# Kernel tuning notes

Measured on AMD Instinct MI355X. Metric: run time of the kernel, lower is better.

The kernel has to match this reference:

```python
import jax, jax.numpy as jnp
import numpy as np

B, S, NH, D_IN = 64, 512, 4, 256   # batch, seq_len, rnn n_head, input_dim
H = 256                            # hidden_dim == attention activation_dim
AH = 256                           # attention_hidden_dim (attn out_dim)
OUT = 3                            # output_dim (sentiment classes)


def setup_inputs() -> dict:
    key = jax.random.key(0)
    ks = jax.random.split(key, 9)
    def p(k, shape, scale=0.05):
        return jax.random.normal(k, shape, dtype=jnp.float32) * scale
    return dict(
        x=jax.random.normal(ks[0], (B, S, NH, D_IN), dtype=jnp.float32),
        Wk=p(ks[1], (D_IN, H)), bk=jnp.zeros((H,), jnp.float32),
        Wq=p(ks[2], (H, H)),    bq=jnp.zeros((H,), jnp.float32),
        w_mlp=p(ks[3], (2 * H,)),
        Wproj=p(ks[4], (H, AH)), bproj=jnp.zeros((AH,), jnp.float32),
        W1=p(ks[5], (D_IN + AH, H)), b1=jnp.zeros((H,), jnp.float32),
        W2=p(ks[6], (H, H)),    b2=jnp.zeros((H,), jnp.float32),
        Wo=p(ks[7], (NH * H, OUT)), bo=jnp.zeros((OUT,), jnp.float32),
    )


def _cell(x_t, hidden, params):
    Wk, bk, Wq, bq, w_mlp, Wproj, bproj, W1, b1, W2, b2, Wo, bo = params
    kx = x_t @ Wk + bk           # [B, NH, H]  keys from step input
    qx = hidden @ Wq + bq        # [B, NH, H]  queries from hidden state
    w1, w2 = w_mlp[:H], w_mlp[H:]
    # MLP score: s[b,i,j] = tanh(cat(kx[b,j], qx[b,i]) . w) = tanh(kx[b,j].w1 + qx[b,i].w2)
    score = jnp.tanh((qx @ w2)[:, :, None] + (kx @ w1)[:, None, :])  # [B, NH, NH]
    score = jax.nn.softmax(score, axis=-1)
    attn = jnp.einsum('bij,bjh->bih', score, kx) @ Wproj + bproj     # [B, NH, AH]
    concat = jnp.concatenate([x_t, attn], axis=-1)                   # [B, NH, D_IN+AH]
    hidden_new = jax.nn.relu(concat @ W1 + b1) @ W2 + b2             # [B, NH, H]
    logits = hidden_new.reshape(B, NH * H) @ Wo + bo                 # [B, OUT]
    out = jax.nn.log_softmax(logits, axis=-1)
    return out, hidden_new


def reference(x, Wk, bk, Wq, bq, w_mlp, Wproj, bproj, W1, b1, W2, b2, Wo, bo):
    params = (Wk, bk, Wq, bq, w_mlp, Wproj, bproj, W1, b1, W2, b2, Wo, bo)
    h0 = jnp.zeros((B, NH, H), x.dtype)
    xs = jnp.swapaxes(x, 0, 1)  # [S, B, NH, D_IN] for scan over time
    def step(h, x_t):
        out, h_new = _cell(x_t, h, params)
        return h_new, out
    h_final, outs = jax.lax.scan(step, h0, xs)
    # return_sequence=False: last-step log-softmax output and final hidden
    return outs[-1], h_final
```

## Files before the change

kernel.cpp:

```cpp
#include <hip/hip_runtime.h>
#include <hip/hip_bf16.h>
#include <math.h>

#define BB   64
#define SS   512
#define NHH  4
#define DD   256
#define HH   256
#define LDH  264

typedef __attribute__((ext_vector_type(8))) short  short8;
typedef __attribute__((ext_vector_type(4))) float  floatx4;


__device__ __forceinline__ unsigned short f2b(float f) {
  __hip_bfloat16 h = __float2bfloat16(f);
  return __builtin_bit_cast(unsigned short, h);
}
__device__ __forceinline__ float b2f(unsigned short u) {
  unsigned v = (unsigned)u << 16;
  return __builtin_bit_cast(float, v);
}

__global__ __launch_bounds__(256) void init_kernel(
    const float* __restrict__ Wk, const float* __restrict__ Wproj,
    const float* __restrict__ W1, const float* __restrict__ Wq,
    const float* __restrict__ bq, const float* __restrict__ w_mlp,
    const float* __restrict__ bproj, const float* __restrict__ W2,
    const float* __restrict__ b2, float* __restrict__ ws,
    unsigned short* __restrict__ wpack)
{
  __shared__ float vsh[256];
  __shared__ float red[256];
  int tid = threadIdx.x;

  if (blockIdx.x > 0) {
    int idx = (blockIdx.x - 1) * 256 + tid;
    int mat = idx >> 16;
    int rem = idx & 65535;
    int j    = rem & 7;
    int lane = (rem >> 3) & 63;
    int ks   = (rem >> 9) & 7;
    int pan  = rem >> 12;
    int k = ks * 32 + ((lane >> 4) << 3) + j;
    int n = pan * 16 + (lane & 15);
    float v;
    if      (mat == 0) v = Wk[k * 256 + n];
    else if (mat == 1) v = W1[k * 256 + n];
    else if (mat == 2) v = Wproj[k * 256 + n];
    else               v = W1[(256 + k) * 256 + n];
    wpack[idx] = f2b(v);
    return;
  }

  const float* w2 = w_mlp + HH;
  {
    float a = 0.f;
    const float4* Wq4 = (const float4*)(Wq + tid * 256);
    const float4* w24 = (const float4*)w2;
    for (int k = 0; k < 64; ++k) {
      float4 wv = Wq4[k], xv = w24[k];
      a = fmaf(wv.x, xv.x, fmaf(wv.y, xv.y, fmaf(wv.z, xv.z, fmaf(wv.w, xv.w, a))));
    }
    vsh[tid] = a;
  }
  __syncthreads();
  {
    float a2 = 0.f;
    const float4* W24 = (const float4*)(W2 + tid * 256);
    const float4* v4  = (const float4*)vsh;
    for (int k = 0; k < 64; ++k) {
      float4 wv = W24[k], xv = v4[k];
      a2 = fmaf(wv.x, xv.x, fmaf(wv.y, xv.y, fmaf(wv.z, xv.z, fmaf(wv.w, xv.w, a2))));
    }
    ws[tid] = a2;
  }
  {
    float a3 = 0.f;
    for (int k = 0; k < 256; ++k) a3 = fmaf(bproj[k], W1[(256 + k) * 256 + tid], a3);
    ws[256 + tid] = a3;
  }
  red[tid] = bq[tid] * w2[tid];
  __syncthreads();
  for (int s = 128; s; s >>= 1) { if (tid < s) red[tid] += red[tid + s]; __syncthreads(); }
  float c = red[0];
  __syncthreads();
  ws[768 + tid] = c;
  red[tid] = b2[tid] * vsh[tid];
  __syncthreads();
  for (int s = 128; s; s >>= 1) { if (tid < s) red[tid] += red[tid + s]; __syncthreads(); }
  if (tid == 0) ws[512] = red[0] + c;
}

__device__ __forceinline__ void mfma_gemm4(
    const unsigned short* A_lds, const short8* __restrict__ Bp,
    const float* __restrict__ bias, floatx4 acc[4][4], int l, int w)
{
  int col = l & 15, quad = l >> 4;
#pragma unroll
  for (int pp = 0; pp < 4; ++pp) {
    float bv = bias ? bias[(w * 4 + pp) * 16 + col] : 0.f;
#pragma unroll
    for (int mf = 0; mf < 4; ++mf)
      acc[mf][pp] = (floatx4){bv, bv, bv, bv};
  }
  const short8* Bb = Bp + (size_t)(w * 4) * 512 + l;
  short8 bb[3][4];
  short8 aa[2][4];
#pragma unroll
  for (int pp = 0; pp < 4; ++pp) bb[0][pp] = Bb[pp * 512];
#pragma unroll
  for (int pp = 0; pp < 4; ++pp) bb[1][pp] = Bb[pp * 512 + 64];
#pragma unroll
  for (int mf = 0; mf < 4; ++mf)
    aa[0][mf] = *(const short8*)(A_lds + (mf * 16 + col) * LDH + quad * 8);
#pragma unroll
  for (int kb = 0; kb < 8; ++kb) {
    if (kb + 2 < 8) {
#pragma unroll
      for (int pp = 0; pp < 4; ++pp)
        bb[(kb + 2) % 3][pp] = Bb[pp * 512 + (kb + 2) * 64];
    }
    if (kb + 1 < 8) {
#pragma unroll
      for (int mf = 0; mf < 4; ++mf)
        aa[(kb + 1) & 1][mf] =
            *(const short8*)(A_lds + (mf * 16 + col) * LDH + (kb + 1) * 32 + quad * 8);
    }
#pragma unroll
    for (int mf = 0; mf < 4; ++mf)
#pragma unroll
      for (int pp = 0; pp < 4; ++pp)
        acc[mf][pp] = __builtin_amdgcn_mfma_f32_16x16x32_bf16(
            aa[kb & 1][mf], bb[kb % 3][pp], acc[mf][pp], 0, 0, 0);
  }
}

__device__ __forceinline__ void acc_to_lds(
    unsigned short* D, const floatx4 acc[4][4], int l, int w)
{
  int col = l & 15, quad = l >> 4;
#pragma unroll
  for (int mf = 0; mf < 4; ++mf)
#pragma unroll
    for (int pp = 0; pp < 4; ++pp)
#pragma unroll
      for (int r = 0; r < 4; ++r)
        D[(mf * 16 + quad * 4 + r) * LDH + (w * 4 + pp) * 16 + col] = f2b(acc[mf][pp][r]);
}

__device__ __forceinline__ void acc_to_global(
    unsigned short* __restrict__ dst, const floatx4 acc[4][4],
    int l, int w, int b, int tt)
{
  int col = l & 15, quad = l >> 4;
#pragma unroll
  for (int mf = 0; mf < 4; ++mf)
#pragma unroll
    for (int r = 0; r < 4; ++r) {
      int m2 = mf * 16 + quad * 4 + r;
      size_t base = (((size_t)(tt * 16 + (m2 >> 2)) * 64 + b) * 4 + (m2 & 3)) * 256;
#pragma unroll
      for (int pp = 0; pp < 4; ++pp)
        dst[base + (w * 4 + pp) * 16 + col] = f2b(acc[mf][pp][r]);
    }
}

__device__ void precompute_block(
    int px, const float* __restrict__ x, const unsigned short* __restrict__ wpack,
    const float* __restrict__ bk, const float* __restrict__ b1,
    const float* __restrict__ w_mlp,
    float* __restrict__ kw_c, unsigned short* __restrict__ xw1_c,
    unsigned short* __restrict__ kpw_c, int t0, char* smem)
{
  float* kwbuf = (float*)smem;
  unsigned short* XS = (unsigned short*)(smem + 2048);
  unsigned short* TS = XS + 64 * LDH;

  int b  = px & 63;
  int tt = px >> 6;
  int tid = threadIdx.x;
  int l = tid & 63, w = tid >> 6;
  int col = l & 15, quad = l >> 4;

  const float4* xsrc = (const float4*)(x + (size_t)(b * SS + t0 + tt * 16) * NHH * DD);
#pragma unroll
  for (int i = 0; i < 16; ++i) {
    int f4 = i * 256 + tid;
    int r = f4 >> 6, c4 = f4 & 63;
    float4 v = xsrc[f4];
    ushort4 h;
    h.x = f2b(v.x); h.y = f2b(v.y); h.z = f2b(v.z); h.w = f2b(v.w);
    *(ushort4*)&XS[r * LDH + c4 * 4] = h;
  }
  __syncthreads();

  const short8* wp0 = (const short8*)(wpack);
  const short8* wp1 = (const short8*)(wpack + 65536);
  const short8* wp2 = (const short8*)(wpack + 2 * 65536);
  const short8* wp3 = (const short8*)(wpack + 3 * 65536);

  floatx4 acc[4][4];

  mfma_gemm4(XS, wp0, bk, acc, l, w);
  acc_to_lds(TS, acc, l, w);
  __syncthreads();

  {
    float part = 0.f;
    const unsigned short* trow = TS + l * LDH + w * 64;
#pragma unroll
    for (int j8 = 0; j8 < 8; ++j8) {
      short8 tv = *(const short8*)(trow + j8 * 8);
#pragma unroll
      for (int j = 0; j < 8; ++j)
        part = fmaf(b2f((unsigned short)tv[j]), w_mlp[w * 64 + j8 * 8 + j], part);
    }
    kwbuf[l * 4 + w] = part;
  }

  mfma_gemm4(XS, wp1, b1, acc, l, w);
  __syncthreads();
  if (tid < 64) {
    float s = kwbuf[tid * 4] + kwbuf[tid * 4 + 1] + kwbuf[tid * 4 + 2] + kwbuf[tid * 4 + 3];
    kw_c[((size_t)(tt * 16 + (tid >> 2)) * 64 + b) * 4 + (tid & 3)] = s;
  }
  acc_to_global(xw1_c, acc, l, w, b, tt);

  mfma_gemm4(TS, wp2, nullptr, acc, l, w);
  acc_to_lds(XS, acc, l, w);
  __syncthreads();

  mfma_gemm4(XS, wp3, nullptr, acc, l, w);
  acc_to_global(kpw_c, acc, l, w, b, tt);
}

__device__ __forceinline__ float wave_reduce_sum(float x) {
#define DPPSTEP(ctrl, rmask)                                                   \
  {                                                                            \
    int _s = __builtin_amdgcn_update_dpp(0, __builtin_bit_cast(int, x),        \
                                         (ctrl), (rmask), 0xf, true);          \
    x += __builtin_bit_cast(float, _s);                                        \
  }
  DPPSTEP(0x111, 0xf)
  DPPSTEP(0x112, 0xf)
  DPPSTEP(0x114, 0xf)
  DPPSTEP(0x118, 0xf)
  DPPSTEP(0x142, 0xa)
  DPPSTEP(0x143, 0xc)
#undef DPPSTEP
  return __builtin_bit_cast(float, __builtin_amdgcn_readlane(__builtin_bit_cast(int, x), 63));
}

__device__ __forceinline__ float tanh_fast(float y) {
  float ex = __expf(2.f * y);
  return 1.f - 2.f * __builtin_amdgcn_rcpf(ex + 1.f);
}

__device__ void seq_block(
    const unsigned short* __restrict__ xw1_c, const unsigned short* __restrict__ kpw_c,
    const float* __restrict__ kw_c, float* __restrict__ ws,
    float* __restrict__ relu_u, int t0, int n)
{
  int b = blockIdx.x;
  int tid = threadIdx.x;
  int i = tid >> 6, l = tid & 63;

  float4 v2v = ((const float4*)ws)[l];
  float4 cbv = ((const float4*)(ws + 256))[l];
  float c2 = ws[512];
  float qw = ws[768 + b * 4 + i];

  const ushort4* xw = (const ushort4*)xw1_c;
  const ushort4* kp = (const ushort4*)kpw_c;

  struct Slot { ushort4 x, k0, k1, k2, k3; float4 kw; };

  auto load = [&](Slot& s, int tc) {
    size_t rb_ = (size_t)(tc * 64 + b) * 4;
    s.x  = xw[(rb_ + i) * 64 + l];
    s.k0 = kp[(rb_ + 0) * 64 + l];
    s.k1 = kp[(rb_ + 1) * 64 + l];
    s.k2 = kp[(rb_ + 2) * 64 + l];
    s.k3 = kp[(rb_ + 3) * 64 + l];
    s.kw = *(const float4*)&kw_c[rb_];
  };

  auto step = [&](Slot& s, int t) {
    float e0 = tanh_fast(qw + s.kw.x);
    float e1 = tanh_fast(qw + s.kw.y);
    float e2 = tanh_fast(qw + s.kw.z);
    float e3 = tanh_fast(qw + s.kw.w);
    float q0 = __expf(e0), q1 = __expf(e1), q2 = __expf(e2), q3 = __expf(e3);
    float inv = __builtin_amdgcn_rcpf(q0 + q1 + q2 + q3);
    float4 K0 = {b2f(s.k0.x), b2f(s.k0.y), b2f(s.k0.z), b2f(s.k0.w)};
    float4 K1 = {b2f(s.k1.x), b2f(s.k1.y), b2f(s.k1.z), b2f(s.k1.w)};
    float4 K2 = {b2f(s.k2.x), b2f(s.k2.y), b2f(s.k2.z), b2f(s.k2.w)};
    float4 K3 = {b2f(s.k3.x), b2f(s.k3.y), b2f(s.k3.z), b2f(s.k3.w)};
    float4 X  = {b2f(s.x.x) + cbv.x, b2f(s.x.y) + cbv.y,
                 b2f(s.x.z) + cbv.z, b2f(s.x.w) + cbv.w};
    float4 a;
    a.x = fmaf(q0, K0.x, fmaf(q1, K1.x, fmaf(q2, K2.x, q3 * K3.x)));
    a.y = fmaf(q0, K0.y, fmaf(q1, K1.y, fmaf(q2, K2.y, q3 * K3.y)));
    a.z = fmaf(q0, K0.z, fmaf(q1, K1.z, fmaf(q2, K2.z, q3 * K3.z)));
    a.w = fmaf(q0, K0.w, fmaf(q1, K1.w, fmaf(q2, K2.w, q3 * K3.w)));
    float4 u;
    u.x = fmaf(a.x, inv, X.x); u.y = fmaf(a.y, inv, X.y);
    u.z = fmaf(a.z, inv, X.z); u.w = fmaf(a.w, inv, X.w);
    float4 r;
    r.x = fmaxf(u.x, 0.f); r.y = fmaxf(u.y, 0.f);
    r.z = fmaxf(u.z, 0.f); r.w = fmaxf(u.w, 0.f);
    float d = fmaf(r.x, v2v.x, fmaf(r.y, v2v.y, fmaf(r.z, v2v.z, r.w * v2v.w)));
    qw = wave_reduce_sum(d) + c2;
    if (t0 + t == SS - 1)
      *(float4*)&relu_u[(size_t)(b * 4 + i) * 256 + l * 4] = r;
  };

  Slot s0, s1, s2, s3;
  load(s0, 0); load(s1, 1); load(s2, 2); load(s3, 3);
  for (int t = 0; t < n; t += 4) {
    int nt;
    step(s0, t);     nt = t + 4; load(s0, nt < n ? nt : n - 1);
    step(s1, t + 1); nt = t + 5; load(s1, nt < n ? nt : n - 1);
    step(s2, t + 2); nt = t + 6; load(s2, nt < n ? nt : n - 1);
    step(s3, t + 3); nt = t + 7; load(s3, nt < n ? nt : n - 1);
  }
  if (l == 0) ws[768 + b * 4 + i] = qw;
}

__global__ __launch_bounds__(256, 2) void fused_kernel(
    const float* __restrict__ x, const unsigned short* __restrict__ wpack,
    const float* __restrict__ bk, const float* __restrict__ b1,
    const float* __restrict__ w_mlp,
    float* kwB, unsigned short* xw1B, unsigned short* kpwB, int t0_pre,
    const float* kwA, const unsigned short* xw1A, const unsigned short* kpwA,
    int t0_seq, int n_seq,
    float* __restrict__ ws, float* __restrict__ relu_u)
{
  __shared__ __align__(16) char smem[2048 + 2 * 64 * LDH * 2];
  if (blockIdx.x < 64) {
    if (n_seq > 0) seq_block(xw1A, kpwA, kwA, ws, relu_u, t0_seq, n_seq);
    return;
  }
  precompute_block(blockIdx.x - 64, x, wpack, bk, b1, w_mlp,
                   kwB, xw1B, kpwB, t0_pre, smem);
}

__global__ __launch_bounds__(256) void final_hidden_kernel(
    const float* __restrict__ relu_u, const float* __restrict__ W2,
    const float* __restrict__ b2, float* __restrict__ out)
{
  __shared__ float rs[256];
  int row = blockIdx.x;
  int tid = threadIdx.x;
  rs[tid] = relu_u[(size_t)row * 256 + tid];
  __syncthreads();
  float acc = b2[tid];
  for (int k = 0; k < 256; ++k) acc = fmaf(rs[k], W2[k * 256 + tid], acc);
  out[192 + (size_t)row * 256 + tid] = acc;
}

__global__ __launch_bounds__(256) void final_logits_kernel(
    const float* __restrict__ hf, const float* __restrict__ Wo,
    const float* __restrict__ bo, float* __restrict__ outp)
{
  __shared__ float r0[256], r1[256], r2[256];
  int b = blockIdx.x;
  int tid = threadIdx.x;
  float a0 = 0.f, a1 = 0.f, a2 = 0.f;
  for (int k = tid; k < 1024; k += 256) {
    float h = hf[(size_t)b * 1024 + k];
    a0 = fmaf(h, Wo[k * 3 + 0], a0);
    a1 = fmaf(h, Wo[k * 3 + 1], a1);
    a2 = fmaf(h, Wo[k * 3 + 2], a2);
  }
  r0[tid] = a0; r1[tid] = a1; r2[tid] = a2;
  __syncthreads();
  for (int s = 128; s; s >>= 1) {
    if (tid < s) { r0[tid] += r0[tid + s]; r1[tid] += r1[tid + s]; r2[tid] += r2[tid + s]; }
    __syncthreads();
  }
  if (tid == 0) {
    float l0 = r0[0] + bo[0], l1 = r1[0] + bo[1], l2 = r2[0] + bo[2];
    float m = fmaxf(l0, fmaxf(l1, l2));
    float lse = m + logf(expf(l0 - m) + expf(l1 - m) + expf(l2 - m));
    outp[b * 3 + 0] = l0 - lse;
    outp[b * 3 + 1] = l1 - lse;
    outp[b * 3 + 2] = l2 - lse;
  }
}

extern "C" void kernel_launch(void* const* d_in, const int* in_sizes, int n_in,
                              void* d_out, int out_size, void* d_ws, size_t ws_size,
                              hipStream_t stream)
{
  const float* x     = (const float*)d_in[0];
  const float* Wk    = (const float*)d_in[1];
  const float* bk    = (const float*)d_in[2];
  const float* Wq    = (const float*)d_in[3];
  const float* bq    = (const float*)d_in[4];
  const float* w_mlp = (const float*)d_in[5];
  const float* Wproj = (const float*)d_in[6];
  const float* bproj = (const float*)d_in[7];
  const float* W1    = (const float*)d_in[8];
  const float* b1    = (const float*)d_in[9];
  const float* W2    = (const float*)d_in[10];
  const float* b2    = (const float*)d_in[11];
  const float* Wo    = (const float*)d_in[12];
  const float* bo    = (const float*)d_in[13];
  float* out = (float*)d_out;
  float* ws  = (float*)d_ws;

  float* ru = ws + 1024;
  unsigned short* wpack = (unsigned short*)(ws + 66560);
  const size_t OFF_CH = 66560 + 131072;
  const long per_t = 256 + 65536;

  long ws_floats = (long)(ws_size / 4);
  long avail = ws_floats - (long)OFF_CH;

  int Tc = 128;
  while (Tc > 0 && 2L * Tc * per_t > avail) Tc -= 16;
  bool pipelined = (Tc >= 16);
  if (!pipelined) {
    Tc = 128;
    while (Tc > 16 && (long)Tc * per_t > avail) Tc -= 16;
  }

  float* bufA = ws + OFF_CH;
  float* bufB = pipelined ? bufA + (size_t)Tc * per_t : bufA;

  auto kw_of  = [&](float* base) { return base; };
  auto xw_of  = [&](float* base) { return (unsigned short*)(base + (size_t)Tc * 256); };
  auto kpw_of = [&](float* base) { return (unsigned short*)(base + (size_t)Tc * 256) + (size_t)Tc * 65536; };

  init_kernel<<<1025, 256, 0, stream>>>(Wk, Wproj, W1, Wq, bq, w_mlp, bproj, W2, b2,
                                        ws, wpack);

  int C = (SS + Tc - 1) / Tc;

  if (pipelined) {
    for (int r = 0; r <= C; ++r) {
      bool hasPre = (r < C);
      bool hasSeq = (r >= 1);
      int t0p = r * Tc;
      int np  = hasPre ? ((SS - t0p) < Tc ? (SS - t0p) : Tc) : 0;
      int t0s = (r - 1) * Tc;
      int ns  = hasSeq ? ((SS - t0s) < Tc ? (SS - t0s) : Tc) : 0;
      float* pB = ((r & 1) ? bufB : bufA);
      float* pA = (((r - 1) & 1) ? bufB : bufA);
      int grid = 64 + (hasPre ? 64 * (np / 16) : 0);
      fused_kernel<<<grid, 256, 0, stream>>>(
          x, wpack, bk, b1, w_mlp,
          kw_of(pB), xw_of(pB), kpw_of(pB), t0p,
          kw_of(pA), xw_of(pA), kpw_of(pA), t0s, ns,
          ws, ru);
    }
  } else {
    for (int c = 0; c < C; ++c) {
      int t0 = c * Tc;
      int n = (SS - t0) < Tc ? (SS - t0) : Tc;
      fused_kernel<<<64 + 64 * (n / 16), 256, 0, stream>>>(
          x, wpack, bk, b1, w_mlp,
          kw_of(bufA), xw_of(bufA), kpw_of(bufA), t0,
          kw_of(bufA), xw_of(bufA), kpw_of(bufA), 0, 0,
          ws, ru);
      fused_kernel<<<64, 256, 0, stream>>>(
          x, wpack, bk, b1, w_mlp,
          kw_of(bufA), xw_of(bufA), kpw_of(bufA), t0,
          kw_of(bufA), xw_of(bufA), kpw_of(bufA), t0, n,
          ws, ru);
    }
  }

  final_hidden_kernel<<<BB * NHH, 256, 0, stream>>>(ru, W2, b2, out);
  final_logits_kernel<<<BB, 256, 0, stream>>>(out + 192, Wo, bo, out);
}
```

Measured before the change: 427.8 us.

## Fold Wk·Wproj·W1b into one fused weight to cut precompute GEMMs

Precomputes the product Wk·Wproj·W1[256:] (and the folded biases and Wk·w1) in new init kernels, so each precompute block runs two MFMA GEMMs on x instead of four chained ones. This also removes the intermediate LDS tile and its syncs, shrinking shared memory enough to raise the occupancy hint to 3 blocks. The A-fragment double buffering in the GEMM loop is dropped in favour of per-iteration loads. Folding three matrices in fp32, then rounding the product to bf16, changes rounding behaviour slightly, and init now costs three launches.

```diff
diff --git a/kernel.cpp b/kernel.cpp
--- a/kernel.cpp
+++ b/kernel.cpp
@@ -12,6 +12,19 @@
 typedef __attribute__((ext_vector_type(8))) short  short8;
 typedef __attribute__((ext_vector_type(4))) float  floatx4;
 
+#define OFF_V2     0
+#define OFF_CB1    256
+#define OFF_C2     512
+#define OFF_CKW    513
+#define OFF_QW     768
+#define OFF_WK1    1024
+#define OFF_BKP    1280
+#define OFF_VT     1536
+#define OFF_RU     1792
+#define OFF_WFUSE  67328
+#define OFF_WKF    132864
+#define OFF_PACK   198400
+#define OFF_CH     263936
 
 __device__ __forceinline__ unsigned short f2b(float f) {
   __hip_bfloat16 h = __float2bfloat16(f);
@@ -22,74 +35,121 @@
   return __builtin_bit_cast(float, v);
 }
 
-__global__ __launch_bounds__(256) void init_kernel(
-    const float* __restrict__ Wk, const float* __restrict__ Wproj,
-    const float* __restrict__ W1, const float* __restrict__ Wq,
-    const float* __restrict__ bq, const float* __restrict__ w_mlp,
-    const float* __restrict__ bproj, const float* __restrict__ W2,
-    const float* __restrict__ b2, float* __restrict__ ws,
-    unsigned short* __restrict__ wpack)
-{
-  __shared__ float vsh[256];
-  __shared__ float red[256];
+__global__ __launch_bounds__(256) void initA_kernel(
+    const float* __restrict__ Wproj, const float* __restrict__ W1,
+    const float* __restrict__ bk, const float* __restrict__ bproj,
+    const float* __restrict__ Wq, const float* __restrict__ w_mlp,
+    float* __restrict__ ws)
+{
   int tid = threadIdx.x;
-
-  if (blockIdx.x > 0) {
-    int idx = (blockIdx.x - 1) * 256 + tid;
-    int mat = idx >> 16;
-    int rem = idx & 65535;
-    int j    = rem & 7;
-    int lane = (rem >> 3) & 63;
-    int ks   = (rem >> 9) & 7;
-    int pan  = rem >> 12;
-    int k = ks * 32 + ((lane >> 4) << 3) + j;
-    int n = pan * 16 + (lane & 15);
-    float v;
-    if      (mat == 0) v = Wk[k * 256 + n];
-    else if (mat == 1) v = W1[k * 256 + n];
-    else if (mat == 2) v = Wproj[k * 256 + n];
-    else               v = W1[(256 + k) * 256 + n];
-    wpack[idx] = f2b(v);
-    return;
-  }
-
-  const float* w2 = w_mlp + HH;
-  {
+  int bx = blockIdx.x;
+  const float* W1b = W1 + 256 * 256;
+  if (bx < 256) {
+    __shared__ float row[256];
+    row[tid] = Wproj[bx * 256 + tid];
+    __syncthreads();
+    float acc = 0.f;
+#pragma unroll 8
+    for (int k = 0; k < 256; ++k)
+      acc = fmaf(row[k], W1b[k * 256 + tid], acc);
+    ws[OFF_WFUSE + bx * 256 + tid] = acc;
+  } else if (bx == 256) {
+    float acc = bproj[tid];
+#pragma unroll 8
+    for (int k = 0; k < 256; ++k)
+      acc = fmaf(bk[k], Wproj[k * 256 + tid], acc);
+    ws[OFF_BKP + tid] = acc;
+  } else {
+    const float4* Wq4 = (const float4*)(Wq + tid * 256);
+    const float4* w24 = (const float4*)(w_mlp + 256);
     float a = 0.f;
-    const float4* Wq4 = (const float4*)(Wq + tid * 256);
-    const float4* w24 = (const float4*)w2;
     for (int k = 0; k < 64; ++k) {
       float4 wv = Wq4[k], xv = w24[k];
       a = fmaf(wv.x, xv.x, fmaf(wv.y, xv.y, fmaf(wv.z, xv.z, fmaf(wv.w, xv.w, a))));
     }
-    vsh[tid] = a;
-  }
-  __syncthreads();
-  {
-    float a2 = 0.f;
-    const float4* W24 = (const float4*)(W2 + tid * 256);
-    const float4* v4  = (const float4*)vsh;
+    ws[OFF_VT + tid] = a;
+  }
+}
+
+__global__ __launch_bounds__(256) void initB_kernel(
+    const float* __restrict__ Wk, const float* __restrict__ W1,
+    const float* __restrict__ b1, const float* __restrict__ W2,
+    const float* __restrict__ b2, const float* __restrict__ bq,
+    const float* __restrict__ bk, const float* __restrict__ w_mlp,
+    float* __restrict__ ws)
+{
+  int tid = threadIdx.x;
+  int bx = blockIdx.x;
+  if (bx < 256) {
+    __shared__ float row[256];
+    row[tid] = Wk[bx * 256 + tid];
+    __syncthreads();
+    float acc = 0.f;
+    const float* Wf = ws + OFF_WFUSE;
+#pragma unroll 8
+    for (int k = 0; k < 256; ++k)
+      acc = fmaf(row[k], Wf[k * 256 + tid], acc);
+    ws[OFF_WKF + bx * 256 + tid] = acc;
+  } else if (bx == 256) {
+    const float* W1b = W1 + 256 * 256;
+    float acc = b1[tid];
+#pragma unroll 8
+    for (int k = 0; k < 256; ++k)
+      acc = fmaf(ws[OFF_BKP + k], W1b[k * 256 + tid], acc);
+    ws[OFF_CB1 + tid] = acc;
+  } else if (bx == 257) {
+    __shared__ float red[256];
+    {
+      const float4* W24 = (const float4*)(W2 + tid * 256);
+      const float4* v4  = (const float4*)(ws + OFF_VT);
+      float a = 0.f;
+      for (int k = 0; k < 64; ++k) {
+        float4 wv = W24[k], xv = v4[k];
+        a = fmaf(wv.x, xv.x, fmaf(wv.y, xv.y, fmaf(wv.z, xv.z, fmaf(wv.w, xv.w, a))));
+      }
+      ws[OFF_V2 + tid] = a;
+    }
+    red[tid] = bq[tid] * w_mlp[256 + tid];
+    __syncthreads();
+    for (int s = 128; s; s >>= 1) { if (tid < s) red[tid] += red[tid + s]; __syncthreads(); }
+    float s2 = red[0];
+    __syncthreads();
+    ws[OFF_QW + tid] = s2;
+    red[tid] = b2[tid] * ws[OFF_VT + tid];
+    __syncthreads();
+    for (int s = 128; s; s >>= 1) { if (tid < s) red[tid] += red[tid + s]; __syncthreads(); }
+    if (tid == 0) ws[OFF_C2] = red[0] + s2;
+    __syncthreads();
+    red[tid] = bk[tid] * w_mlp[tid];
+    __syncthreads();
+    for (int s = 128; s; s >>= 1) { if (tid < s) red[tid] += red[tid + s]; __syncthreads(); }
+    if (tid == 0) ws[OFF_CKW] = red[0];
+  } else {
+    const float4* Wk4 = (const float4*)(Wk + tid * 256);
+    const float4* w14 = (const float4*)(w_mlp);
+    float a = 0.f;
     for (int k = 0; k < 64; ++k) {
-      float4 wv = W24[k], xv = v4[k];
-      a2 = fmaf(wv.x, xv.x, fmaf(wv.y, xv.y, fmaf(wv.z, xv.z, fmaf(wv.w, xv.w, a2))));
-    }
-    ws[tid] = a2;
-  }
-  {
-    float a3 = 0.f;
-    for (int k = 0; k < 256; ++k) a3 = fmaf(bproj[k], W1[(256 + k) * 256 + tid], a3);
-    ws[256 + tid] = a3;
-  }
-  red[tid] = bq[tid] * w2[tid];
-  __syncthreads();
-  for (int s = 128; s; s >>= 1) { if (tid < s) red[tid] += red[tid + s]; __syncthreads(); }
-  float c = red[0];
-  __syncthreads();
-  ws[768 + tid] = c;
-  red[tid] = b2[tid] * vsh[tid];
-  __syncthreads();
-  for (int s = 128; s; s >>= 1) { if (tid < s) red[tid] += red[tid + s]; __syncthreads(); }
-  if (tid == 0) ws[512] = red[0] + c;
+      float4 wv = Wk4[k], xv = w14[k];
+      a = fmaf(wv.x, xv.x, fmaf(wv.y, xv.y, fmaf(wv.z, xv.z, fmaf(wv.w, xv.w, a))));
+    }
+    ws[OFF_WK1 + tid] = a;
+  }
+}
+
+__global__ __launch_bounds__(256) void initC_kernel(
+    const float* __restrict__ W1, float* __restrict__ ws)
+{
+  int idx = blockIdx.x * 256 + threadIdx.x;
+  int mat = idx >> 16;
+  int rem = idx & 65535;
+  int j    = rem & 7;
+  int lane = (rem >> 3) & 63;
+  int ks   = (rem >> 9) & 7;
+  int pan  = rem >> 12;
+  int k = ks * 32 + ((lane >> 4) << 3) + j;
+  int n = pan * 16 + (lane & 15);
+  float v = (mat == 0) ? ws[OFF_WKF + k * 256 + n] : W1[k * 256 + n];
+  ((unsigned short*)(ws + OFF_PACK))[idx] = f2b(v);
 }
 
 __device__ __forceinline__ void mfma_gemm4(
@@ -106,14 +166,10 @@
   }
   const short8* Bb = Bp + (size_t)(w * 4) * 512 + l;
   short8 bb[3][4];
-  short8 aa[2][4];
 #pragma unroll
   for (int pp = 0; pp < 4; ++pp) bb[0][pp] = Bb[pp * 512];
 #pragma unroll
   for (int pp = 0; pp < 4; ++pp) bb[1][pp] = Bb[pp * 512 + 64];
-#pragma unroll
-  for (int mf = 0; mf < 4; ++mf)
-    aa[0][mf] = *(const short8*)(A_lds + (mf * 16 + col) * LDH + quad * 8);
 #pragma unroll
   for (int kb = 0; kb < 8; ++kb) {
     if (kb + 2 < 8) {
@@ -121,32 +177,17 @@
       for (int pp = 0; pp < 4; ++pp)
         bb[(kb + 2) % 3][pp] = Bb[pp * 512 + (kb + 2) * 64];
     }
-    if (kb + 1 < 8) {
-#pragma unroll
-      for (int mf = 0; mf < 4; ++mf)
-        aa[(kb + 1) & 1][mf] =
-            *(const short8*)(A_lds + (mf * 16 + col) * LDH + (kb + 1) * 32 + quad * 8);
-    }
+    short8 aa[4];
+#pragma unroll
+    for (int mf = 0; mf < 4; ++mf)
+      aa[mf] = *(const short8*)(A_lds + (mf * 16 + col) * LDH + kb * 32 + quad * 8);
 #pragma unroll
     for (int mf = 0; mf < 4; ++mf)
 #pragma unroll
       for (int pp = 0; pp < 4; ++pp)
         acc[mf][pp] = __builtin_amdgcn_mfma_f32_16x16x32_bf16(
-            aa[kb & 1][mf], bb[kb % 3][pp], acc[mf][pp], 0, 0, 0);
-  }
-}
-
-__device__ __forceinline__ void acc_to_lds(
-    unsigned short* D, const floatx4 acc[4][4], int l, int w)
-{
-  int col = l & 15, quad = l >> 4;
-#pragma unroll
-  for (int mf = 0; mf < 4; ++mf)
-#pragma unroll
-    for (int pp = 0; pp < 4; ++pp)
-#pragma unroll
-      for (int r = 0; r < 4; ++r)
-        D[(mf * 16 + quad * 4 + r) * LDH + (w * 4 + pp) * 16 + col] = f2b(acc[mf][pp][r]);
+            aa[mf], bb[kb % 3][pp], acc[mf][pp], 0, 0, 0);
+  }
 }
 
 __device__ __forceinline__ void acc_to_global(
@@ -167,21 +208,15 @@
 }
 
 __device__ void precompute_block(
-    int px, const float* __restrict__ x, const unsigned short* __restrict__ wpack,
-    const float* __restrict__ bk, const float* __restrict__ b1,
-    const float* __restrict__ w_mlp,
+    int px, const float* __restrict__ x, const float* __restrict__ ws,
     float* __restrict__ kw_c, unsigned short* __restrict__ xw1_c,
-    unsigned short* __restrict__ kpw_c, int t0, char* smem)
-{
-  float* kwbuf = (float*)smem;
-  unsigned short* XS = (unsigned short*)(smem + 2048);
-  unsigned short* TS = XS + 64 * LDH;
-
+    unsigned short* __restrict__ kpw_c, int t0,
+    float* kwbuf, unsigned short* XS)
+{
   int b  = px & 63;
   int tt = px >> 6;
   int tid = threadIdx.x;
   int l = tid & 63, w = tid >> 6;
-  int col = l & 15, quad = l >> 4;
 
   const float4* xsrc = (const float4*)(x + (size_t)(b * SS + t0 + tt * 16) * NHH * DD);
 #pragma unroll
@@ -195,44 +230,36 @@
   }
   __syncthreads();
 
-  const short8* wp0 = (const short8*)(wpack);
-  const short8* wp1 = (const short8*)(wpack + 65536);
-  const short8* wp2 = (const short8*)(wpack + 2 * 65536);
-  const short8* wp3 = (const short8*)(wpack + 3 * 65536);
-
-  floatx4 acc[4][4];
-
-  mfma_gemm4(XS, wp0, bk, acc, l, w);
-  acc_to_lds(TS, acc, l, w);
-  __syncthreads();
+  const short8* wp0 = (const short8*)((const unsigned short*)(ws + OFF_PACK));
+  const short8* wp1 = (const short8*)((const unsigned short*)(ws + OFF_PACK) + 65536);
 
   {
     float part = 0.f;
-    const unsigned short* trow = TS + l * LDH + w * 64;
+    const unsigned short* trow = XS + l * LDH + w * 64;
 #pragma unroll
     for (int j8 = 0; j8 < 8; ++j8) {
       short8 tv = *(const short8*)(trow + j8 * 8);
 #pragma unroll
       for (int j = 0; j < 8; ++j)
-        part = fmaf(b2f((unsigned short)tv[j]), w_mlp[w * 64 + j8 * 8 + j], part);
+        part = fmaf(b2f((unsigned short)tv[j]), ws[OFF_WK1 + w * 64 + j8 * 8 + j], part);
     }
     kwbuf[l * 4 + w] = part;
   }
 
-  mfma_gemm4(XS, wp1, b1, acc, l, w);
+  floatx4 acc[4][4];
+
+  mfma_gemm4(XS, wp0, nullptr, acc, l, w);
+  acc_to_global(kpw_c, acc, l, w, b, tt);
   __syncthreads();
+
   if (tid < 64) {
-    float s = kwbuf[tid * 4] + kwbuf[tid * 4 + 1] + kwbuf[tid * 4 + 2] + kwbuf[tid * 4 + 3];
+    float s = kwbuf[tid * 4] + kwbuf[tid * 4 + 1] + kwbuf[tid * 4 + 2] + kwbuf[tid * 4 + 3]
+            + ws[OFF_CKW];
     kw_c[((size_t)(tt * 16 + (tid >> 2)) * 64 + b) * 4 + (tid & 3)] = s;
   }
+
+  mfma_gemm4(XS, wp1, ws + OFF_CB1, acc, l, w);
   acc_to_global(xw1_c, acc, l, w, b, tt);
-
-  mfma_gemm4(TS, wp2, nullptr, acc, l, w);
-  acc_to_lds(XS, acc, l, w);
-  __syncthreads();
-
-  mfma_gemm4(XS, wp3, nullptr, acc, l, w);
-  acc_to_global(kpw_c, acc, l, w, b, tt);
 }
 
 __device__ __forceinline__ float wave_reduce_sum(float x) {
@@ -266,10 +293,9 @@
   int tid = threadIdx.x;
   int i = tid >> 6, l = tid & 63;
 
-  float4 v2v = ((const float4*)ws)[l];
-  float4 cbv = ((const float4*)(ws + 256))[l];
-  float c2 = ws[512];
-  float qw = ws[768 + b * 4 + i];
+  float4 v2v = ((const float4*)(ws + OFF_V2))[l];
+  float c2 = ws[OFF_C2];
+  float qw = ws[OFF_QW + b * 4 + i];
 
   const ushort4* xw = (const ushort4*)xw1_c;
   const ushort4* kp = (const ushort4*)kpw_c;
@@ -297,8 +323,7 @@
     float4 K1 = {b2f(s.k1.x), b2f(s.k1.y), b2f(s.k1.z), b2f(s.k1.w)};
     float4 K2 = {b2f(s.k2.x), b2f(s.k2.y), b2f(s.k2.z), b2f(s.k2.w)};
     float4 K3 = {b2f(s.k3.x), b2f(s.k3.y), b2f(s.k3.z), b2f(s.k3.w)};
-    float4 X  = {b2f(s.x.x) + cbv.x, b2f(s.x.y) + cbv.y,
-                 b2f(s.x.z) + cbv.z, b2f(s.x.w) + cbv.w};
+    float4 X  = {b2f(s.x.x), b2f(s.x.y), b2f(s.x.z), b2f(s.x.w)};
     float4 a;
     a.x = fmaf(q0, K0.x, fmaf(q1, K1.x, fmaf(q2, K2.x, q3 * K3.x)));
     a.y = fmaf(q0, K0.y, fmaf(q1, K1.y, fmaf(q2, K2.y, q3 * K3.y)));
@@ -325,25 +350,23 @@
     step(s2, t + 2); nt = t + 6; load(s2, nt < n ? nt : n - 1);
     step(s3, t + 3); nt = t + 7; load(s3, nt < n ? nt : n - 1);
   }
-  if (l == 0) ws[768 + b * 4 + i] = qw;
-}
-
-__global__ __launch_bounds__(256, 2) void fused_kernel(
-    const float* __restrict__ x, const unsigned short* __restrict__ wpack,
-    const float* __restrict__ bk, const float* __restrict__ b1,
-    const float* __restrict__ w_mlp,
+  if (l == 0) ws[OFF_QW + b * 4 + i] = qw;
+}
+
+__global__ __launch_bounds__(256, 3) void fused_kernel(
+    const float* __restrict__ x,
     float* kwB, unsigned short* xw1B, unsigned short* kpwB, int t0_pre,
     const float* kwA, const unsigned short* xw1A, const unsigned short* kpwA,
     int t0_seq, int n_seq,
     float* __restrict__ ws, float* __restrict__ relu_u)
 {
-  __shared__ __align__(16) char smem[2048 + 2 * 64 * LDH * 2];
+  __shared__ float kwbuf[256];
+  __shared__ __align__(16) unsigned short XS[64 * LDH];
   if (blockIdx.x < 64) {
     if (n_seq > 0) seq_block(xw1A, kpwA, kwA, ws, relu_u, t0_seq, n_seq);
     return;
   }
-  precompute_block(blockIdx.x - 64, x, wpack, bk, b1, w_mlp,
-                   kwB, xw1B, kpwB, t0_pre, smem);
+  precompute_block(blockIdx.x - 64, x, ws, kwB, xw1B, kpwB, t0_pre, kwbuf, XS);
 }
 
 __global__ __launch_bounds__(256) void final_hidden_kernel(
@@ -411,9 +434,7 @@
   float* out = (float*)d_out;
   float* ws  = (float*)d_ws;
 
-  float* ru = ws + 1024;
-  unsigned short* wpack = (unsigned short*)(ws + 66560);
-  const size_t OFF_CH = 66560 + 131072;
+  float* ru = ws + OFF_RU;
   const long per_t = 256 + 65536;
 
   long ws_floats = (long)(ws_size / 4);
@@ -434,8 +455,9 @@
   auto xw_of  = [&](float* base) { return (unsigned short*)(base + (size_t)Tc * 256); };
   auto kpw_of = [&](float* base) { return (unsigned short*)(base + (size_t)Tc * 256) + (size_t)Tc * 65536; };
 
-  init_kernel<<<1025, 256, 0, stream>>>(Wk, Wproj, W1, Wq, bq, w_mlp, bproj, W2, b2,
-                                        ws, wpack);
+  initA_kernel<<<258, 256, 0, stream>>>(Wproj, W1, bk, bproj, Wq, w_mlp, ws);
+  initB_kernel<<<259, 256, 0, stream>>>(Wk, W1, b1, W2, b2, bq, bk, w_mlp, ws);
+  initC_kernel<<<512, 256, 0, stream>>>(W1, ws);
 
   int C = (SS + Tc - 1) / Tc;
 
@@ -451,7 +473,7 @@
       float* pA = (((r - 1) & 1) ? bufB : bufA);
       int grid = 64 + (hasPre ? 64 * (np / 16) : 0);
       fused_kernel<<<grid, 256, 0, stream>>>(
-          x, wpack, bk, b1, w_mlp,
+          x,
           kw_of(pB), xw_of(pB), kpw_of(pB), t0p,
           kw_of(pA), xw_of(pA), kpw_of(pA), t0s, ns,
           ws, ru);
@@ -461,12 +483,12 @@
       int t0 = c * Tc;
       int n = (SS - t0) < Tc ? (SS - t0) : Tc;
       fused_kernel<<<64 + 64 * (n / 16), 256, 0, stream>>>(
-          x, wpack, bk, b1, w_mlp,
+          x,
           kw_of(bufA), xw_of(bufA), kpw_of(bufA), t0,
           kw_of(bufA), xw_of(bufA), kpw_of(bufA), 0, 0,
           ws, ru);
       fused_kernel<<<64, 256, 0, stream>>>(
-          x, wpack, bk, b1, w_mlp,
+          x,
           kw_of(bufA), xw_of(bufA), kpw_of(bufA), t0,
           kw_of(bufA), xw_of(bufA), kpw_of(bufA), t0, n,
           ws, ru);
```

Result: no change. 434.9 us (+1.7%).
